# Kernel tuning notes

Measured on AMD Instinct MI355X. Metric: run time of the kernel, lower is better.

Reference implementation:

```python
import jax, jax.numpy as jnp
import numpy as np
from jax import lax

NUM_TAGS = 126
T = NUM_TAGS + 2          # tag_size = 128
B, S = 256, 512
START, STOP = T - 3, T - 2
NEG = -10000.0


def setup_inputs() -> dict:
    key = jax.random.key(0)
    k1, k2, k3 = jax.random.split(key, 3)
    feats = jax.random.normal(k1, (B, S, T), jnp.float32)
    # learned transition matrix with the module's init masking pattern
    trans = jax.random.normal(k2, (T, T), jnp.float32)
    trans = trans.at[:, START].set(NEG).at[STOP, :].set(NEG)
    trans = trans.at[:, 0].set(NEG).at[0, :].set(NEG)
    # prefix masks with varying valid lengths in [S/2, S]
    lengths = jax.random.randint(k3, (B,), S // 2, S + 1)
    mask = jnp.arange(S)[None, :] < lengths[:, None]
    return {"feats": feats, "mask": mask, "transitions": trans}


def reference(feats, mask, transitions):
    # Viterbi decode (module.forward returns (None, decode_idx)).
    Bn, Sn, Tn = feats.shape
    start, stop = Tn - 3, Tn - 2
    emit = jnp.transpose(feats, (1, 0, 2))            # (S, B, T)
    m = jnp.transpose(mask.astype(jnp.int32))         # (S, B)
    lengths = mask.astype(jnp.int32).sum(axis=1)      # (B,)

    part0 = emit[0] + transitions[start][None, :]     # (B, T)

    def step(part, inp):
        e_t, m_t = inp
        # scores[t, b, i, j] = feats[t, b, j] + transitions[i, j]
        cur = part[:, :, None] + transitions[None, :, :] + e_t[:, None, :]  # (B, from, to)
        new_part = cur.max(axis=1)                                          # (B, T)
        bp = jnp.argmax(cur, axis=1).astype(jnp.int32)                      # (B, T)
        bp = jnp.where(m_t[:, None] > 0, bp, 0)
        return new_part, (new_part, bp)

    _, (hist, bps) = lax.scan(step, part0, (emit[1:], m[1:]))
    part_hist = jnp.concatenate([part0[None], hist], axis=0)                # (S, B, T)
    back_points = jnp.concatenate(
        [bps, jnp.zeros((1, Bn, Tn), jnp.int32)], axis=0)                   # (S, B, T)

    bidx = jnp.arange(Bn)
    last_pos = lengths - 1                                                  # (B,)
    last_partition = part_hist[last_pos, bidx]                              # (B, T)
    last_bp = jnp.argmax(last_partition[:, :, None] + transitions[None], axis=1)
    pointer = last_bp[:, stop].astype(jnp.int32)                            # (B,)

    # overwrite back_points at the last valid position with the final pointer
    bp_bt = jnp.transpose(back_points, (1, 0, 2))                           # (B, S, T)
    bp_bt = bp_bt.at[bidx, last_pos].set(
        jnp.broadcast_to(pointer[:, None], (Bn, Tn)))
    back_points = jnp.transpose(bp_bt, (1, 0, 2))                           # (S, B, T)

    def trace(ptr, bp_t):
        new_ptr = jnp.take_along_axis(bp_t, ptr[:, None], axis=1)[:, 0]
        return new_ptr, new_ptr

    _, rev = lax.scan(trace, pointer, back_points[:-1], reverse=True)       # (S-1, B)
    decode = jnp.concatenate([rev, pointer[None]], axis=0)                  # (S, B)
    return jnp.transpose(decode)                                            # (B, S)
```

## Files before the change

### kernel.cpp

```cpp
#include <hip/hip_runtime.h>
#include <cstdint>
#include <cstddef>

constexpr int T_ = 128;
constexpr int S_ = 512;
constexpr int B_ = 256;
constexpr int START_ = T_ - 3;
constexpr int STOP_  = T_ - 2;

__device__ __forceinline__ void lds_barrier() {
  asm volatile("s_waitcnt lgkmcnt(0)\n\ts_barrier" ::: "memory");
}

__device__ __forceinline__ float readlane_f(float v, int sl) {
  return __int_as_float(__builtin_amdgcn_readlane(__float_as_int(v), sl));
}

__device__ __forceinline__ float ig16_rmax(float m) {
  int x = __builtin_amdgcn_mov_dpp(__float_as_int(m), 0xB1, 0xF, 0xF, true);
  m = fmaxf(m, __int_as_float(x));
  x = __builtin_amdgcn_mov_dpp(__float_as_int(m), 0x4E, 0xF, 0xF, true);
  m = fmaxf(m, __int_as_float(x));
  x = __builtin_amdgcn_mov_dpp(__float_as_int(m), 0x141, 0xF, 0xF, true);
  m = fmaxf(m, __int_as_float(x));
  x = __builtin_amdgcn_mov_dpp(__float_as_int(m), 0x140, 0xF, 0xF, true);
  m = fmaxf(m, __int_as_float(x));
  return m;
}

__global__ __launch_bounds__(512, 2) void viterbi_forward(
    const float* __restrict__ feats,
    const float* __restrict__ trans,
    float* __restrict__ ph)
{
  const int b    = blockIdx.x;
  const int tid  = threadIdx.x;
  const int lane = tid & 63;
  const int ig   = lane & 15;
  const int jg   = tid >> 4;
  const int j0   = jg * 4;

  __shared__ alignas(16) float part[2][192];

  float4 tc[8];
  #pragma unroll
  for (int ii = 0; ii < 8; ++ii)
    tc[ii] = *(const float4*)&trans[(8 * ig + ii) * T_ + j0];

  const float* fb = feats + (size_t)b * S_ * T_;
  const int woff  = j0 + 4 * (j0 >> 3);

  float4 e0 = *(const float4*)&fb[j0];
  float4 ts = *(const float4*)&trans[START_ * T_ + j0];
  float4 p0 = make_float4(e0.x + ts.x, e0.y + ts.y, e0.z + ts.z, e0.w + ts.w);
  if (ig == 0) {
    *(float4*)&part[0][woff] = p0;
    *(float4*)&ph[(size_t)b * T_ + j0] = p0;
  }
  __syncthreads();

  auto stepf = [&](int t, float4 e4) {
    const float4* p4 = (const float4*)part[(t - 1) & 1];
    float4 pa = p4[3 * ig];
    float4 pb = p4[3 * ig + 1];
    const float pv[8] = {pa.x, pa.y, pa.z, pa.w, pb.x, pb.y, pb.z, pb.w};
    float m[4];
    #pragma unroll
    for (int c = 0; c < 4; ++c) {
      float a0 = pv[0] + ((const float*)&tc[0])[c];
      float a1 = pv[1] + ((const float*)&tc[1])[c];
      float a2 = pv[2] + ((const float*)&tc[2])[c];
      float a3 = pv[3] + ((const float*)&tc[3])[c];
      float a4 = pv[4] + ((const float*)&tc[4])[c];
      float a5 = pv[5] + ((const float*)&tc[5])[c];
      float a6 = pv[6] + ((const float*)&tc[6])[c];
      float a7 = pv[7] + ((const float*)&tc[7])[c];
      float mm = fmaxf(fmaxf(fmaxf(a0, a1), fmaxf(a2, a3)),
                       fmaxf(fmaxf(a4, a5), fmaxf(a6, a7)));
      m[c] = ig16_rmax(mm);
    }
    float4 np4 = make_float4(m[0] + e4.x, m[1] + e4.y, m[2] + e4.z, m[3] + e4.w);
    if (ig == 0) *(float4*)&part[t & 1][woff] = np4;
    lds_barrier();
    if (ig == 0)
      *(float4*)&ph[((size_t)t * B_ + b) * T_ + j0] = np4;
  };

  float4 EA[4], EB[4];
  #pragma unroll
  for (int u = 0; u < 4; ++u)
    EA[u] = *(const float4*)&fb[(size_t)(1 + u) * T_ + j0];

  for (int t0 = 1; t0 < S_; t0 += 8) {
    #pragma unroll
    for (int u = 0; u < 4; ++u) {
      int tr = t0 + 4 + u; if (tr > S_ - 1) tr = S_ - 1;
      EB[u] = *(const float4*)&fb[(size_t)tr * T_ + j0];
    }
    #pragma unroll
    for (int u = 0; u < 4; ++u) { int t = t0 + u; if (t < S_) stepf(t, EA[u]); }
    #pragma unroll
    for (int u = 0; u < 4; ++u) {
      int tr = t0 + 8 + u; if (tr > S_ - 1) tr = S_ - 1;
      EA[u] = *(const float4*)&fb[(size_t)tr * T_ + j0];
    }
    #pragma unroll
    for (int u = 0; u < 4; ++u) { int t = t0 + 4 + u; if (t < S_) stepf(t, EB[u]); }
  }
}

constexpr int CH_ = 8;
constexpr int TS_ = 130;

__global__ __launch_bounds__(64, 1) void viterbi_trace(
    const float* __restrict__ feats,
    const void*  __restrict__ mask,
    const float* __restrict__ trans,
    const float* __restrict__ ph,
    int* __restrict__ out)
{
  const int b    = blockIdx.x;
  const int lane = threadIdx.x;

  __shared__ alignas(16) float transT[T_ * TS_];
  #pragma unroll 4
  for (int g = lane; g < T_ * T_; g += 64) {
    int i = g >> 7, jj = g & (T_ - 1);
    transT[jj * TS_ + i] = trans[g];
  }
  __syncthreads();

  int len = 0;
  {
    const int w0 = *(const int*)mask;
    if (w0 == 0x01010101) {
      const unsigned char* m = (const unsigned char*)mask + (size_t)b * S_;
      for (int s = lane; s < S_; s += 64) len += (m[s] != 0);
    } else if (w0 == 0x3F800000) {
      const float* m = (const float*)mask + (size_t)b * S_;
      for (int s = lane; s < S_; s += 64) len += (m[s] != 0.0f);
    } else {
      const int* m = (const int*)mask + (size_t)b * S_;
      for (int s = lane; s < S_; s += 64) len += (m[s] != 0);
    }
    #pragma unroll
    for (int o = 32; o > 0; o >>= 1) len += __shfl_xor(len, o);
  }
  const int lp = len - 1;

  const float2 L = *(const float2*)(ph + ((size_t)lp * B_ + b) * T_ + 2 * lane);
  float v0 = L.x + transT[STOP_ * TS_ + 2 * lane];
  float v1 = L.y + transT[STOP_ * TS_ + 2 * lane + 1];
  float mx = fmaxf(v0, v1);
  #pragma unroll
  for (int o = 32; o > 0; o >>= 1) mx = fmaxf(mx, __shfl_xor(mx, o));
  {
    unsigned long long g0 = __ballot(v0 == mx);
    unsigned long long g1 = __ballot(v1 == mx);
    int p0 = g0 ? 2 * (__ffsll(g0) - 1)     : (1 << 30);
    int p1 = g1 ? 2 * (__ffsll(g1) - 1) + 1 : (1 << 30);
    int pointer = min(p0, p1);

    for (int k = lp + 1 + lane; k <= S_ - 2; k += 64) out[b * S_ + k] = 0;
    if (lane == 0) {
      out[b * S_ + (S_ - 1)] = pointer;
      if (lp < S_ - 1) out[b * S_ + lp] = pointer;
    }

    int   ptr = pointer;
    float tg  = readlane_f((ptr & 1) ? L.y : L.x, ptr >> 1);
    const float* fb = feats + (size_t)b * S_ * T_;
    const float2 FL = *(const float2*)(fb + (size_t)lp * T_ + 2 * lane);
    float e = readlane_f((ptr & 1) ? FL.y : FL.x, ptr >> 1);

    float2 PA[CH_], FA[CH_], PB[CH_], FB[CH_];

    auto issue = [&](float2 (&P)[CH_], float2 (&F)[CH_], int k0) {
      #pragma unroll
      for (int s = 0; s < CH_; ++s) {
        int k = k0 - s; if (k < 0) k = 0;
        P[s] = *(const float2*)(ph + ((size_t)k * B_ + b) * T_ + 2 * lane);
        F[s] = *(const float2*)(fb + (size_t)k * T_ + 2 * lane);
      }
    };
    auto process = [&](const float2 (&P)[CH_], const float2 (&F)[CH_], int k0) {
      #pragma unroll
      for (int s = 0; s < CH_; ++s) {
        const int k = k0 - s;
        if (k >= 0) {
          const float2 tr = *(const float2*)(transT + ptr * TS_ + 2 * lane);
          float cx = (P[s].x + tr.x) + e;
          float cy = (P[s].y + tr.y) + e;
          unsigned long long q0 = __ballot(cx == tg);
          unsigned long long q1 = __ballot(cy == tg);
          int a0 = q0 ? 2 * (__ffsll(q0) - 1)     : (1 << 30);
          int a1 = q1 ? 2 * (__ffsll(q1) - 1) + 1 : (1 << 30);
          ptr = min(a0, a1);
          if (lane == 0) out[b * S_ + k] = ptr;
          tg = readlane_f((ptr & 1) ? P[s].y : P[s].x, ptr >> 1);
          e  = readlane_f((ptr & 1) ? F[s].y : F[s].x, ptr >> 1);
        }
      }
    };

    issue(PA, FA, lp - 1);
    for (int k0 = lp - 1; k0 >= 0; k0 -= 2 * CH_) {
      issue(PB, FB, k0 - CH_);
      process(PA, FA, k0);
      issue(PA, FA, k0 - 2 * CH_);
      process(PB, FB, k0 - CH_);
    }
  }
}

extern "C" void kernel_launch(void* const* d_in, const int* in_sizes, int n_in,
                              void* d_out, int out_size, void* d_ws, size_t ws_size,
                              hipStream_t stream) {
  const float* feats = (const float*)d_in[0];
  const void*  mask  = d_in[1];
  const float* trans = (const float*)d_in[2];
  float* ph = (float*)d_ws;
  int*   out = (int*)d_out;

  viterbi_forward<<<dim3(B_), dim3(512), 0, stream>>>(feats, trans, ph);
  viterbi_trace  <<<dim3(B_), dim3(64), 0, stream>>>(feats, mask, trans, ph, out);
}
```

Measured before the change: 414.7 us.

## Widen forward to 1024 threads, batch-major history, LDS-staged traceback windows

The forward kernel now runs 1024 threads per block, with each thread handling two output tags instead of four. This halves the per-step serial max work but doubles the number of waves meeting at every barrier. The partition history is stored batch-major, so each batch's rows are contiguous. The traceback kernel now copies 16-step windows of history and emissions into double-buffered LDS with coalesced float4 loads, replacing per-step strided global loads, at the cost of extra LDS and copy work.

```diff
diff --git a/kernel.cpp b/kernel.cpp
--- a/kernel.cpp
+++ b/kernel.cpp
@@ -11,6 +11,9 @@
 __device__ __forceinline__ void lds_barrier() {
   asm volatile("s_waitcnt lgkmcnt(0)\n\ts_barrier" ::: "memory");
 }
+__device__ __forceinline__ void lgkm_wait() {
+  asm volatile("s_waitcnt lgkmcnt(0)" ::: "memory");
+}
 
 __device__ __forceinline__ float readlane_f(float v, int sl) {
   return __int_as_float(__builtin_amdgcn_readlane(__float_as_int(v), sl));
@@ -28,7 +31,7 @@
   return m;
 }
 
-__global__ __launch_bounds__(512, 2) void viterbi_forward(
+__global__ __launch_bounds__(1024, 4) void viterbi_forward(
     const float* __restrict__ feats,
     const float* __restrict__ trans,
     float* __restrict__ ph)
@@ -38,79 +41,82 @@
   const int lane = tid & 63;
   const int ig   = lane & 15;
   const int jg   = tid >> 4;
-  const int j0   = jg * 4;
+  const int j0   = jg * 2;
 
   __shared__ alignas(16) float part[2][192];
 
-  float4 tc[8];
+  float2 tc[8];
   #pragma unroll
   for (int ii = 0; ii < 8; ++ii)
-    tc[ii] = *(const float4*)&trans[(8 * ig + ii) * T_ + j0];
-
-  const float* fb = feats + (size_t)b * S_ * T_;
-  const int woff  = j0 + 4 * (j0 >> 3);
-
-  float4 e0 = *(const float4*)&fb[j0];
-  float4 ts = *(const float4*)&trans[START_ * T_ + j0];
-  float4 p0 = make_float4(e0.x + ts.x, e0.y + ts.y, e0.z + ts.z, e0.w + ts.w);
+    tc[ii] = *(const float2*)&trans[(8 * ig + ii) * T_ + j0];
+
+  const float* fb  = feats + (size_t)b * S_ * T_;
+  float*       phb = ph    + (size_t)b * S_ * T_;
+  const int woff   = j0 + 4 * (j0 >> 3);
+
+  float2 e0 = *(const float2*)&fb[j0];
+  float2 ts = *(const float2*)&trans[START_ * T_ + j0];
+  float2 p0 = {e0.x + ts.x, e0.y + ts.y};
   if (ig == 0) {
-    *(float4*)&part[0][woff] = p0;
-    *(float4*)&ph[(size_t)b * T_ + j0] = p0;
+    *(float2*)&part[0][woff] = p0;
+    *(float2*)&phb[j0] = p0;
   }
   __syncthreads();
 
-  auto stepf = [&](int t, float4 e4) {
+  auto stepf = [&](int t, float2 e2) {
     const float4* p4 = (const float4*)part[(t - 1) & 1];
     float4 pa = p4[3 * ig];
     float4 pb = p4[3 * ig + 1];
     const float pv[8] = {pa.x, pa.y, pa.z, pa.w, pb.x, pb.y, pb.z, pb.w};
-    float m[4];
-    #pragma unroll
-    for (int c = 0; c < 4; ++c) {
-      float a0 = pv[0] + ((const float*)&tc[0])[c];
-      float a1 = pv[1] + ((const float*)&tc[1])[c];
-      float a2 = pv[2] + ((const float*)&tc[2])[c];
-      float a3 = pv[3] + ((const float*)&tc[3])[c];
-      float a4 = pv[4] + ((const float*)&tc[4])[c];
-      float a5 = pv[5] + ((const float*)&tc[5])[c];
-      float a6 = pv[6] + ((const float*)&tc[6])[c];
-      float a7 = pv[7] + ((const float*)&tc[7])[c];
-      float mm = fmaxf(fmaxf(fmaxf(a0, a1), fmaxf(a2, a3)),
-                       fmaxf(fmaxf(a4, a5), fmaxf(a6, a7)));
-      m[c] = ig16_rmax(mm);
-    }
-    float4 np4 = make_float4(m[0] + e4.x, m[1] + e4.y, m[2] + e4.z, m[3] + e4.w);
-    if (ig == 0) *(float4*)&part[t & 1][woff] = np4;
+    float m0, m1;
+    {
+      float a0 = pv[0] + tc[0].x, a1 = pv[1] + tc[1].x;
+      float a2 = pv[2] + tc[2].x, a3 = pv[3] + tc[3].x;
+      float a4 = pv[4] + tc[4].x, a5 = pv[5] + tc[5].x;
+      float a6 = pv[6] + tc[6].x, a7 = pv[7] + tc[7].x;
+      m0 = ig16_rmax(fmaxf(fmaxf(fmaxf(a0, a1), fmaxf(a2, a3)),
+                           fmaxf(fmaxf(a4, a5), fmaxf(a6, a7))));
+    }
+    {
+      float a0 = pv[0] + tc[0].y, a1 = pv[1] + tc[1].y;
+      float a2 = pv[2] + tc[2].y, a3 = pv[3] + tc[3].y;
+      float a4 = pv[4] + tc[4].y, a5 = pv[5] + tc[5].y;
+      float a6 = pv[6] + tc[6].y, a7 = pv[7] + tc[7].y;
+      m1 = ig16_rmax(fmaxf(fmaxf(fmaxf(a0, a1), fmaxf(a2, a3)),
+                           fmaxf(fmaxf(a4, a5), fmaxf(a6, a7))));
+    }
+    float2 np = {m0 + e2.x, m1 + e2.y};
+    if (ig == 0) *(float2*)&part[t & 1][woff] = np;
     lds_barrier();
     if (ig == 0)
-      *(float4*)&ph[((size_t)t * B_ + b) * T_ + j0] = np4;
+      *(float2*)&phb[(size_t)t * T_ + j0] = np;
   };
 
-  float4 EA[4], EB[4];
+  float2 EA[4], EB[4];
   #pragma unroll
   for (int u = 0; u < 4; ++u)
-    EA[u] = *(const float4*)&fb[(size_t)(1 + u) * T_ + j0];
+    EA[u] = *(const float2*)&fb[(size_t)(1 + u) * T_ + j0];
 
   for (int t0 = 1; t0 < S_; t0 += 8) {
     #pragma unroll
     for (int u = 0; u < 4; ++u) {
       int tr = t0 + 4 + u; if (tr > S_ - 1) tr = S_ - 1;
-      EB[u] = *(const float4*)&fb[(size_t)tr * T_ + j0];
+      EB[u] = *(const float2*)&fb[(size_t)tr * T_ + j0];
     }
     #pragma unroll
     for (int u = 0; u < 4; ++u) { int t = t0 + u; if (t < S_) stepf(t, EA[u]); }
     #pragma unroll
     for (int u = 0; u < 4; ++u) {
       int tr = t0 + 8 + u; if (tr > S_ - 1) tr = S_ - 1;
-      EA[u] = *(const float4*)&fb[(size_t)tr * T_ + j0];
+      EA[u] = *(const float2*)&fb[(size_t)tr * T_ + j0];
     }
     #pragma unroll
     for (int u = 0; u < 4; ++u) { int t = t0 + 4 + u; if (t < S_) stepf(t, EB[u]); }
   }
 }
 
-constexpr int CH_ = 8;
 constexpr int TS_ = 130;
+constexpr int WS_ = 16;
 
 __global__ __launch_bounds__(64, 1) void viterbi_trace(
     const float* __restrict__ feats,
@@ -123,6 +129,9 @@
   const int lane = threadIdx.x;
 
   __shared__ alignas(16) float transT[T_ * TS_];
+  __shared__ alignas(16) float phs[2][WS_ * T_];
+  __shared__ alignas(16) float fes[2][WS_ * T_];
+
   #pragma unroll 4
   for (int g = lane; g < T_ * T_; g += 64) {
     int i = g >> 7, jj = g & (T_ - 1);
@@ -132,11 +141,11 @@
 
   int len = 0;
   {
-    const int w0 = *(const int*)mask;
-    if (w0 == 0x01010101) {
+    const int w0m = *(const int*)mask;
+    if (w0m == 0x01010101) {
       const unsigned char* m = (const unsigned char*)mask + (size_t)b * S_;
       for (int s = lane; s < S_; s += 64) len += (m[s] != 0);
-    } else if (w0 == 0x3F800000) {
+    } else if (w0m == 0x3F800000) {
       const float* m = (const float*)mask + (size_t)b * S_;
       for (int s = lane; s < S_; s += 64) len += (m[s] != 0.0f);
     } else {
@@ -148,68 +157,82 @@
   }
   const int lp = len - 1;
 
-  const float2 L = *(const float2*)(ph + ((size_t)lp * B_ + b) * T_ + 2 * lane);
+  const float* phb = ph    + (size_t)b * S_ * T_;
+  const float* fb  = feats + (size_t)b * S_ * T_;
+
+  const float2 L = *(const float2*)(phb + (size_t)lp * T_ + 2 * lane);
   float v0 = L.x + transT[STOP_ * TS_ + 2 * lane];
   float v1 = L.y + transT[STOP_ * TS_ + 2 * lane + 1];
   float mx = fmaxf(v0, v1);
   #pragma unroll
   for (int o = 32; o > 0; o >>= 1) mx = fmaxf(mx, __shfl_xor(mx, o));
-  {
-    unsigned long long g0 = __ballot(v0 == mx);
-    unsigned long long g1 = __ballot(v1 == mx);
-    int p0 = g0 ? 2 * (__ffsll(g0) - 1)     : (1 << 30);
-    int p1 = g1 ? 2 * (__ffsll(g1) - 1) + 1 : (1 << 30);
-    int pointer = min(p0, p1);
-
-    for (int k = lp + 1 + lane; k <= S_ - 2; k += 64) out[b * S_ + k] = 0;
-    if (lane == 0) {
-      out[b * S_ + (S_ - 1)] = pointer;
-      if (lp < S_ - 1) out[b * S_ + lp] = pointer;
-    }
-
-    int   ptr = pointer;
-    float tg  = readlane_f((ptr & 1) ? L.y : L.x, ptr >> 1);
-    const float* fb = feats + (size_t)b * S_ * T_;
-    const float2 FL = *(const float2*)(fb + (size_t)lp * T_ + 2 * lane);
-    float e = readlane_f((ptr & 1) ? FL.y : FL.x, ptr >> 1);
-
-    float2 PA[CH_], FA[CH_], PB[CH_], FB[CH_];
-
-    auto issue = [&](float2 (&P)[CH_], float2 (&F)[CH_], int k0) {
-      #pragma unroll
-      for (int s = 0; s < CH_; ++s) {
-        int k = k0 - s; if (k < 0) k = 0;
-        P[s] = *(const float2*)(ph + ((size_t)k * B_ + b) * T_ + 2 * lane);
-        F[s] = *(const float2*)(fb + (size_t)k * T_ + 2 * lane);
-      }
-    };
-    auto process = [&](const float2 (&P)[CH_], const float2 (&F)[CH_], int k0) {
-      #pragma unroll
-      for (int s = 0; s < CH_; ++s) {
-        const int k = k0 - s;
-        if (k >= 0) {
-          const float2 tr = *(const float2*)(transT + ptr * TS_ + 2 * lane);
-          float cx = (P[s].x + tr.x) + e;
-          float cy = (P[s].y + tr.y) + e;
-          unsigned long long q0 = __ballot(cx == tg);
-          unsigned long long q1 = __ballot(cy == tg);
-          int a0 = q0 ? 2 * (__ffsll(q0) - 1)     : (1 << 30);
-          int a1 = q1 ? 2 * (__ffsll(q1) - 1) + 1 : (1 << 30);
-          ptr = min(a0, a1);
-          if (lane == 0) out[b * S_ + k] = ptr;
-          tg = readlane_f((ptr & 1) ? P[s].y : P[s].x, ptr >> 1);
-          e  = readlane_f((ptr & 1) ? F[s].y : F[s].x, ptr >> 1);
-        }
-      }
-    };
-
-    issue(PA, FA, lp - 1);
-    for (int k0 = lp - 1; k0 >= 0; k0 -= 2 * CH_) {
-      issue(PB, FB, k0 - CH_);
-      process(PA, FA, k0);
-      issue(PA, FA, k0 - 2 * CH_);
-      process(PB, FB, k0 - CH_);
-    }
+  unsigned long long g0 = __ballot(v0 == mx);
+  unsigned long long g1 = __ballot(v1 == mx);
+  int p0 = g0 ? 2 * (__ffsll(g0) - 1)     : (1 << 30);
+  int p1 = g1 ? 2 * (__ffsll(g1) - 1) + 1 : (1 << 30);
+  const int pointer = min(p0, p1);
+
+  for (int k = lp + 1 + lane; k <= S_ - 2; k += 64) out[b * S_ + k] = 0;
+  if (lane == 0) {
+    out[b * S_ + (S_ - 1)] = pointer;
+    if (lp < S_ - 1) out[b * S_ + lp] = pointer;
+  }
+
+  int   ptr = pointer;
+  float tg  = readlane_f((ptr & 1) ? L.y : L.x, ptr >> 1);
+  const float2 FL = *(const float2*)(fb + (size_t)lp * T_ + 2 * lane);
+  float e = readlane_f((ptr & 1) ? FL.y : FL.x, ptr >> 1);
+
+  float4 RP[8], RF[8];
+
+  auto load_regs = [&](int w) {
+    const float4* gp = (const float4*)(phb + (size_t)(WS_ * w) * T_);
+    const float4* gf = (const float4*)(fb  + (size_t)(WS_ * w) * T_);
+    #pragma unroll
+    for (int q = 0; q < 8; ++q) {
+      RP[q] = gp[q * 64 + lane];
+      RF[q] = gf[q * 64 + lane];
+    }
+  };
+  auto write_lds = [&](int buf) {
+    float4* dp = (float4*)phs[buf];
+    float4* df = (float4*)fes[buf];
+    #pragma unroll
+    for (int q = 0; q < 8; ++q) {
+      dp[q * 64 + lane] = RP[q];
+      df[q * 64 + lane] = RF[q];
+    }
+    lgkm_wait();
+  };
+
+  const int w0 = (lp - 1) >> 4;
+  load_regs(w0);
+  write_lds(0);
+  int cur = 0;
+  int khi = lp - 1;
+  for (int w = w0; w >= 0; --w) {
+    if (w > 0) load_regs(w - 1);
+    const int klo = WS_ * w;
+    const float* Prow = phs[cur];
+    const float* Frow = fes[cur];
+    for (int k = khi; k >= klo; --k) {
+      const int r = k - klo;
+      const float2 P  = *(const float2*)(Prow + r * T_ + 2 * lane);
+      const float2 tr = *(const float2*)(transT + ptr * TS_ + 2 * lane);
+      float cx = (P.x + tr.x) + e;
+      float cy = (P.y + tr.y) + e;
+      unsigned long long q0 = __ballot(cx == tg);
+      unsigned long long q1 = __ballot(cy == tg);
+      int a0 = q0 ? 2 * (__ffsll(q0) - 1)     : (1 << 30);
+      int a1 = q1 ? 2 * (__ffsll(q1) - 1) + 1 : (1 << 30);
+      ptr = min(a0, a1);
+      if (lane == 0) out[b * S_ + k] = ptr;
+      tg = readlane_f((ptr & 1) ? P.y : P.x, ptr >> 1);
+      e  = Frow[r * T_ + ptr];
+    }
+    if (w > 0) write_lds(cur ^ 1);
+    cur ^= 1;
+    khi = klo - 1;
   }
 }
 
@@ -222,6 +245,6 @@
   float* ph = (float*)d_ws;
   int*   out = (int*)d_out;
 
-  viterbi_forward<<<dim3(B_), dim3(512), 0, stream>>>(feats, trans, ph);
+  viterbi_forward<<<dim3(B_), dim3(1024), 0, stream>>>(feats, trans, ph);
   viterbi_trace  <<<dim3(B_), dim3(64), 0, stream>>>(feats, mask, trans, ph, out);
 }
```

After: 440.1 us. 1.06x slower.

## Split forward Viterbi step across 1024 threads with packed float2 math

Applied to the files above, without the earlier changes.

The forward kernel goes from 512 to 1024 threads per block, so each 16-lane group handles 2 destination tags instead of 4. The max reductions use packed 2-wide vector max and paired DPP moves. The partition history layout changes from time-major to batch-major, making each block's writes and the trace kernel's reads contiguous per sequence, and the step loop is restructured with pointer increments and a peeled tail. The aim is to shorten the serial per-step critical path, at the cost of more waves taking part in every per-step barrier.

```diff
diff --git a/kernel.cpp b/kernel.cpp
--- a/kernel.cpp
+++ b/kernel.cpp
@@ -8,6 +8,8 @@
 constexpr int START_ = T_ - 3;
 constexpr int STOP_  = T_ - 2;
 
+typedef float f32x2 __attribute__((ext_vector_type(2)));
+
 __device__ __forceinline__ void lds_barrier() {
   asm volatile("s_waitcnt lgkmcnt(0)\n\ts_barrier" ::: "memory");
 }
@@ -16,19 +18,26 @@
   return __int_as_float(__builtin_amdgcn_readlane(__float_as_int(v), sl));
 }
 
-__device__ __forceinline__ float ig16_rmax(float m) {
-  int x = __builtin_amdgcn_mov_dpp(__float_as_int(m), 0xB1, 0xF, 0xF, true);
-  m = fmaxf(m, __int_as_float(x));
-  x = __builtin_amdgcn_mov_dpp(__float_as_int(m), 0x4E, 0xF, 0xF, true);
-  m = fmaxf(m, __int_as_float(x));
-  x = __builtin_amdgcn_mov_dpp(__float_as_int(m), 0x141, 0xF, 0xF, true);
-  m = fmaxf(m, __int_as_float(x));
-  x = __builtin_amdgcn_mov_dpp(__float_as_int(m), 0x140, 0xF, 0xF, true);
-  m = fmaxf(m, __int_as_float(x));
+__device__ __forceinline__ f32x2 max2(f32x2 a, f32x2 b) {
+  return __builtin_elementwise_max(a, b);
+}
+
+template <int CTRL>
+__device__ __forceinline__ f32x2 dpp_max2(f32x2 m) {
+  int lo = __builtin_amdgcn_mov_dpp(__float_as_int(m.x), CTRL, 0xF, 0xF, true);
+  int hi = __builtin_amdgcn_mov_dpp(__float_as_int(m.y), CTRL, 0xF, 0xF, true);
+  f32x2 o; o.x = __int_as_float(lo); o.y = __int_as_float(hi);
+  return max2(m, o);
+}
+__device__ __forceinline__ f32x2 ig16_rmax2(f32x2 m) {
+  m = dpp_max2<0xB1>(m);
+  m = dpp_max2<0x4E>(m);
+  m = dpp_max2<0x141>(m);
+  m = dpp_max2<0x140>(m);
   return m;
 }
 
-__global__ __launch_bounds__(512, 2) void viterbi_forward(
+__global__ __launch_bounds__(1024, 4) void viterbi_forward(
     const float* __restrict__ feats,
     const float* __restrict__ trans,
     float* __restrict__ ph)
@@ -38,74 +47,85 @@
   const int lane = tid & 63;
   const int ig   = lane & 15;
   const int jg   = tid >> 4;
-  const int j0   = jg * 4;
+  const int j0   = jg * 2;
 
   __shared__ alignas(16) float part[2][192];
 
-  float4 tc[8];
-  #pragma unroll
-  for (int ii = 0; ii < 8; ++ii)
-    tc[ii] = *(const float4*)&trans[(8 * ig + ii) * T_ + j0];
-
-  const float* fb = feats + (size_t)b * S_ * T_;
-  const int woff  = j0 + 4 * (j0 >> 3);
-
-  float4 e0 = *(const float4*)&fb[j0];
-  float4 ts = *(const float4*)&trans[START_ * T_ + j0];
-  float4 p0 = make_float4(e0.x + ts.x, e0.y + ts.y, e0.z + ts.z, e0.w + ts.w);
+  f32x2 tcp[2][4];
+  #pragma unroll
+  for (int a = 0; a < 4; ++a) {
+    f32x2 r0 = *(const f32x2*)&trans[(8 * ig + 2 * a)     * T_ + j0];
+    f32x2 r1 = *(const f32x2*)&trans[(8 * ig + 2 * a + 1) * T_ + j0];
+    tcp[0][a].x = r0.x; tcp[0][a].y = r1.x;
+    tcp[1][a].x = r0.y; tcp[1][a].y = r1.y;
+  }
+
+  const float* fb  = feats + (size_t)b * S_ * T_;
+  float*       phb = ph    + (size_t)b * S_ * T_;
+  const int woff   = j0 + 4 * (j0 >> 3);
+
+  f32x2 e0 = *(const f32x2*)&fb[j0];
+  f32x2 ts = *(const f32x2*)&trans[START_ * T_ + j0];
+  f32x2 p0 = e0 + ts;
   if (ig == 0) {
-    *(float4*)&part[0][woff] = p0;
-    *(float4*)&ph[(size_t)b * T_ + j0] = p0;
+    *(f32x2*)&part[0][woff] = p0;
+    *(f32x2*)&phb[j0] = p0;
   }
   __syncthreads();
 
-  auto stepf = [&](int t, float4 e4) {
-    const float4* p4 = (const float4*)part[(t - 1) & 1];
+  auto stepf = [&](const float* rbuf, float* wbuf, float* phrow, f32x2 e2) {
+    const float4* p4 = (const float4*)rbuf;
     float4 pa = p4[3 * ig];
     float4 pb = p4[3 * ig + 1];
-    const float pv[8] = {pa.x, pa.y, pa.z, pa.w, pb.x, pb.y, pb.z, pb.w};
-    float m[4];
-    #pragma unroll
-    for (int c = 0; c < 4; ++c) {
-      float a0 = pv[0] + ((const float*)&tc[0])[c];
-      float a1 = pv[1] + ((const float*)&tc[1])[c];
-      float a2 = pv[2] + ((const float*)&tc[2])[c];
-      float a3 = pv[3] + ((const float*)&tc[3])[c];
-      float a4 = pv[4] + ((const float*)&tc[4])[c];
-      float a5 = pv[5] + ((const float*)&tc[5])[c];
-      float a6 = pv[6] + ((const float*)&tc[6])[c];
-      float a7 = pv[7] + ((const float*)&tc[7])[c];
-      float mm = fmaxf(fmaxf(fmaxf(a0, a1), fmaxf(a2, a3)),
-                       fmaxf(fmaxf(a4, a5), fmaxf(a6, a7)));
-      m[c] = ig16_rmax(mm);
-    }
-    float4 np4 = make_float4(m[0] + e4.x, m[1] + e4.y, m[2] + e4.z, m[3] + e4.w);
-    if (ig == 0) *(float4*)&part[t & 1][woff] = np4;
+    f32x2 pv0 = {pa.x, pa.y}, pv1 = {pa.z, pa.w};
+    f32x2 pv2 = {pb.x, pb.y}, pv3 = {pb.z, pb.w};
+    f32x2 m01;
+    {
+      f32x2 mm = max2(max2(pv0 + tcp[0][0], pv1 + tcp[0][1]),
+                      max2(pv2 + tcp[0][2], pv3 + tcp[0][3]));
+      m01.x = fmaxf(mm.x, mm.y);
+    }
+    {
+      f32x2 mm = max2(max2(pv0 + tcp[1][0], pv1 + tcp[1][1]),
+                      max2(pv2 + tcp[1][2], pv3 + tcp[1][3]));
+      m01.y = fmaxf(mm.x, mm.y);
+    }
+    f32x2 np = ig16_rmax2(m01) + e2;
+    if (ig == 0) *(f32x2*)&part[0][(wbuf - part[0]) + woff] = np;
     lds_barrier();
-    if (ig == 0)
-      *(float4*)&ph[((size_t)t * B_ + b) * T_ + j0] = np4;
+    if (ig == 0) *(f32x2*)&phrow[j0] = np;
   };
 
-  float4 EA[4], EB[4];
-  #pragma unroll
-  for (int u = 0; u < 4; ++u)
-    EA[u] = *(const float4*)&fb[(size_t)(1 + u) * T_ + j0];
-
-  for (int t0 = 1; t0 < S_; t0 += 8) {
+  f32x2 EA[4], EB[4];
+  const float* pf = fb + j0 + T_;
+  #pragma unroll
+  for (int u = 0; u < 4; ++u) { EA[u] = *(const f32x2*)pf; pf += T_; }
+
+  float* phrow = phb + T_;
+  for (int tb = 0; tb < 63; ++tb) {
+    #pragma unroll
+    for (int u = 0; u < 4; ++u) { EB[u] = *(const f32x2*)pf; pf += T_; }
     #pragma unroll
     for (int u = 0; u < 4; ++u) {
-      int tr = t0 + 4 + u; if (tr > S_ - 1) tr = S_ - 1;
-      EB[u] = *(const float4*)&fb[(size_t)tr * T_ + j0];
-    }
-    #pragma unroll
-    for (int u = 0; u < 4; ++u) { int t = t0 + u; if (t < S_) stepf(t, EA[u]); }
+      stepf(part[u & 1], part[(u + 1) & 1], phrow, EA[u]); phrow += T_;
+    }
+    #pragma unroll
+    for (int u = 0; u < 4; ++u) { EA[u] = *(const f32x2*)pf; pf += T_; }
     #pragma unroll
     for (int u = 0; u < 4; ++u) {
-      int tr = t0 + 8 + u; if (tr > S_ - 1) tr = S_ - 1;
-      EA[u] = *(const float4*)&fb[(size_t)tr * T_ + j0];
-    }
-    #pragma unroll
-    for (int u = 0; u < 4; ++u) { int t = t0 + 4 + u; if (t < S_) stepf(t, EB[u]); }
+      stepf(part[u & 1], part[(u + 1) & 1], phrow, EB[u]); phrow += T_;
+    }
+  }
+  f32x2 ET[3];
+  #pragma unroll
+  for (int u = 0; u < 3; ++u) { ET[u] = *(const f32x2*)pf; pf += T_; }
+  #pragma unroll
+  for (int u = 0; u < 4; ++u) {
+    stepf(part[u & 1], part[(u + 1) & 1], phrow, EA[u]); phrow += T_;
+  }
+  #pragma unroll
+  for (int u = 0; u < 3; ++u) {
+    stepf(part[u & 1], part[(u + 1) & 1], phrow, ET[u]); phrow += T_;
   }
 }
 
@@ -132,11 +152,11 @@
 
   int len = 0;
   {
-    const int w0 = *(const int*)mask;
-    if (w0 == 0x01010101) {
+    const int w0m = *(const int*)mask;
+    if (w0m == 0x01010101) {
       const unsigned char* m = (const unsigned char*)mask + (size_t)b * S_;
       for (int s = lane; s < S_; s += 64) len += (m[s] != 0);
-    } else if (w0 == 0x3F800000) {
+    } else if (w0m == 0x3F800000) {
       const float* m = (const float*)mask + (size_t)b * S_;
       for (int s = lane; s < S_; s += 64) len += (m[s] != 0.0f);
     } else {
@@ -148,7 +168,10 @@
   }
   const int lp = len - 1;
 
-  const float2 L = *(const float2*)(ph + ((size_t)lp * B_ + b) * T_ + 2 * lane);
+  const float* phb = ph    + (size_t)b * S_ * T_;
+  const float* fb  = feats + (size_t)b * S_ * T_;
+
+  const float2 L = *(const float2*)(phb + (size_t)lp * T_ + 2 * lane);
   float v0 = L.x + transT[STOP_ * TS_ + 2 * lane];
   float v1 = L.y + transT[STOP_ * TS_ + 2 * lane + 1];
   float mx = fmaxf(v0, v1);
@@ -169,7 +192,6 @@
 
     int   ptr = pointer;
     float tg  = readlane_f((ptr & 1) ? L.y : L.x, ptr >> 1);
-    const float* fb = feats + (size_t)b * S_ * T_;
     const float2 FL = *(const float2*)(fb + (size_t)lp * T_ + 2 * lane);
     float e = readlane_f((ptr & 1) ? FL.y : FL.x, ptr >> 1);
 
@@ -179,8 +201,8 @@
       #pragma unroll
       for (int s = 0; s < CH_; ++s) {
         int k = k0 - s; if (k < 0) k = 0;
-        P[s] = *(const float2*)(ph + ((size_t)k * B_ + b) * T_ + 2 * lane);
-        F[s] = *(const float2*)(fb + (size_t)k * T_ + 2 * lane);
+        P[s] = *(const float2*)(phb + (size_t)k * T_ + 2 * lane);
+        F[s] = *(const float2*)(fb  + (size_t)k * T_ + 2 * lane);
       }
     };
     auto process = [&](const float2 (&P)[CH_], const float2 (&F)[CH_], int k0) {
@@ -222,6 +244,6 @@
   float* ph = (float*)d_ws;
   int*   out = (int*)d_out;
 
-  viterbi_forward<<<dim3(B_), dim3(512), 0, stream>>>(feats, trans, ph);
+  viterbi_forward<<<dim3(B_), dim3(1024), 0, stream>>>(feats, trans, ph);
   viterbi_trace  <<<dim3(B_), dim3(64), 0, stream>>>(feats, mask, trans, ph, out);
 }
```

Result: no change. 421.4 us (+1.6%).
